# Optimization experiments

Measured on AMD Instinct MI355X. Metric: run time of the kernel, lower is better.

Reference implementation:

```python
import jax, jax.numpy as jnp
import numpy as np

B, T, D, Q = 32, 2048, 512, 512


def setup_inputs() -> dict:
    key = jax.random.key(0)
    k0, k1, k2, k3, k4, k5 = jax.random.split(key, 6)
    output_data = jax.random.normal(k0, (B, T, D), dtype=jnp.float32)
    query = jax.random.normal(k1, (B, Q), dtype=jnp.float32)
    # valid lengths in [1, T] so no row is fully masked
    lengths = jax.random.randint(k2, (B,), 1, T + 1).astype(jnp.int32)
    w = jax.random.normal(k3, (D, D), dtype=jnp.float32) * (1.0 / np.sqrt(D))
    u = jax.random.normal(k4, (D, Q), dtype=jnp.float32) * (1.0 / np.sqrt(Q))
    v = jax.random.normal(k5, (D, 1), dtype=jnp.float32)
    return {"output_data": output_data, "query": query, "lengths": lengths,
            "w": w, "u": u, "v": v}


def reference(output_data, query, lengths, w, u, v):
    # raw_score = W @ output + U @ query (broadcast over seq)   [B, T, D]
    raw = jnp.einsum('btd,ed->bte', output_data, w) \
        + jnp.einsum('bq,eq->be', query, u)[:, None, :]
    # score = tanh(raw) @ v                                     [B, T, 1]
    score = jnp.tanh(raw) @ v
    # additive mask: 0 on valid positions, -inf on padding
    valid = jnp.arange(T)[None, :] < lengths[:, None]           # [B, T]
    score = score + jnp.where(valid, 0.0, -jnp.inf)[:, :, None]
    weights = jax.nn.softmax(score, axis=1)                     # [B, T, 1]
    expectation = jnp.sum(weights * output_data, axis=1)        # [B, D]
    # dropout_rate=0.0 -> dropout is identity
    return score, weights, expectation
```

## Files before the change

kernel.cpp:

```cpp
#include <hip/hip_runtime.h>
#include <math.h>


#define TPB 256
constexpr int B = 32, T = 2048, D = 512, Qd = 512;
constexpr int NROW = B * T;
#define NEG_SENTINEL (-1e30f)

typedef __attribute__((ext_vector_type(8))) short bf16x8;
typedef __attribute__((ext_vector_type(4))) float f32x4;

__device__ __forceinline__ unsigned rne16(float f) {
    unsigned u = __builtin_bit_cast(unsigned, f);
    return (u + 0x7FFFu + ((u >> 16) & 1u)) >> 16;
}
__device__ __forceinline__ unsigned packsplit(float f0, float f1, unsigned& lopack) {
    unsigned h0 = rne16(f0), h1 = rne16(f1);
    float r0 = f0 - __builtin_bit_cast(float, h0 << 16);
    float r1 = f1 - __builtin_bit_cast(float, h1 << 16);
    lopack = rne16(r0) | (rne16(r1) << 16);
    return h0 | (h1 << 16);
}
__device__ __forceinline__ void cvt8(const float4 a, const float4 b, uint4& hi, uint4& lo) {
    hi.x = packsplit(a.x, a.y, lo.x);
    hi.y = packsplit(a.z, a.w, lo.y);
    hi.z = packsplit(b.x, b.y, lo.z);
    hi.w = packsplit(b.z, b.w, lo.w);
}

__global__ void k_uq(const float* __restrict__ query, const float* __restrict__ u,
                     float* __restrict__ uq) {
    int b = blockIdx.x;
    __shared__ float q_s[Qd];
    for (int i = threadIdx.x; i < Qd; i += TPB) q_s[i] = query[b * Qd + i];
    __syncthreads();
    for (int e = threadIdx.x; e < D; e += TPB) {
        const float4* urow = (const float4*)(u + (size_t)e * Qd);
        float acc = 0.f;
        for (int q4 = 0; q4 < Qd / 4; ++q4) {
            float4 uu = urow[q4];
            float4 qq = *(const float4*)(q_s + q4 * 4);
            acc += uu.x * qq.x + uu.y * qq.y + uu.z * qq.z + uu.w * qq.w;
        }
        uq[b * D + e] = acc;
    }
}

__global__ void k_convW(const float* __restrict__ W,
                        uint4* __restrict__ WhF, uint4* __restrict__ WlF) {
    const int g = blockIdx.x * 256 + threadIdx.x;
    const int e = g >> 6, s = g & 63;
    const float4* src = (const float4*)(W + (size_t)e * D + s * 8);
    float4 a = src[0], bq = src[1];
    uint4 hi, lo;
    cvt8(a, bq, hi, lo);
    const int nt = e >> 7, cb = (e >> 4) & 7, lo16 = e & 15;
    const int kc = s >> 2, hi4 = s & 3;
    const size_t idx = ((size_t)(nt * 16 + kc) * 8 + cb) * 64 + hi4 * 16 + lo16;
    WhF[idx] = hi;
    WlF[idx] = lo;
}

__global__ __launch_bounds__(256, 2) void k_gemm(
    const float* __restrict__ X,
    const uint4* __restrict__ WhF,
    const uint4* __restrict__ WlF,
    const float* __restrict__ v,
    const float* __restrict__ uqg,
    float* __restrict__ partialS)
{
    __shared__ uint4 Ah[4 * 128], Al[4 * 128];
    __shared__ float scr[2][128];

    const int gidx = blockIdx.x;
    const int logical = (gidx & 7) * 256 + (gidx >> 3);
    const int mt = logical >> 2, nt = logical & 3;
    const int row0 = mt * 128, e0 = nt * 128;
    const int b = row0 >> 11;

    const int tid = threadIdx.x, lane = tid & 63, wid = tid >> 6;
    const int wm = wid >> 1, wn = wid & 1;
    const int lo16 = lane & 15, hi4 = lane >> 4;
    const int arow = tid & 127, akh = tid >> 7;

    const float4* Xg = (const float4*)(X + (size_t)(row0 + arow) * D + akh * 16);
    const uint4* WhB = WhF + ((size_t)nt * 16) * 8 * 64 + (wn * 4) * 64 + lane;
    const uint4* WlB = WlF + ((size_t)nt * 16) * 8 * 64 + (wn * 4) * 64 + lane;

    f32x4 acc[4][4];
#pragma unroll
    for (int i = 0; i < 4; ++i)
#pragma unroll
        for (int j = 0; j < 4; ++j) acc[i][j] = (f32x4){0.f, 0.f, 0.f, 0.f};

    float4 xr0 = Xg[0], xr1 = Xg[1], xr2 = Xg[2], xr3 = Xg[3];

    for (int kc = 0; kc < 16; ++kc) {
        __syncthreads();
        uint4 bhr[4], blr[4];
        {
            const uint4* wh = WhB + (size_t)kc * 8 * 64;
            const uint4* wl = WlB + (size_t)kc * 8 * 64;
#pragma unroll
            for (int fc = 0; fc < 4; ++fc) {
                bhr[fc] = wh[fc * 64];
                blr[fc] = wl[fc * 64];
            }
        }
        {
            uint4 hp, lp;
            cvt8(xr0, xr1, hp, lp);
            Ah[(akh * 2 + 0) * 128 + arow] = hp;
            Al[(akh * 2 + 0) * 128 + arow] = lp;
            cvt8(xr2, xr3, hp, lp);
            Ah[(akh * 2 + 1) * 128 + arow] = hp;
            Al[(akh * 2 + 1) * 128 + arow] = lp;
        }
        __syncthreads();

        bf16x8 aH[4], aL[4];
#pragma unroll
        for (int fr = 0; fr < 4; ++fr) {
            const int idx = hi4 * 128 + wm * 64 + fr * 16 + lo16;
            aH[fr] = __builtin_bit_cast(bf16x8, Ah[idx]);
            aL[fr] = __builtin_bit_cast(bf16x8, Al[idx]);
        }
        if (kc + 1 < 16) {
            const float4* xn = Xg + (size_t)(kc + 1) * 8;
            xr0 = xn[0]; xr1 = xn[1]; xr2 = xn[2]; xr3 = xn[3];
        }
#pragma unroll
        for (int fc = 0; fc < 4; ++fc) {
            const bf16x8 bH = __builtin_bit_cast(bf16x8, bhr[fc]);
            const bf16x8 bL = __builtin_bit_cast(bf16x8, blr[fc]);
#pragma unroll
            for (int fr = 0; fr < 4; ++fr) {
                acc[fr][fc] = __builtin_amdgcn_mfma_f32_16x16x32_bf16(aH[fr], bH, acc[fr][fc], 0, 0, 0);
                acc[fr][fc] = __builtin_amdgcn_mfma_f32_16x16x32_bf16(aH[fr], bL, acc[fr][fc], 0, 0, 0);
                acc[fr][fc] = __builtin_amdgcn_mfma_f32_16x16x32_bf16(aL[fr], bH, acc[fr][fc], 0, 0, 0);
            }
        }
    }

    const int colbase = e0 + wn * 64;
#pragma unroll
    for (int fr = 0; fr < 4; ++fr) {
        float ps[4] = {0.f, 0.f, 0.f, 0.f};
#pragma unroll
        for (int fc = 0; fc < 4; ++fc) {
            const int col = colbase + fc * 16 + lo16;
            const float uqc = uqg[b * D + col];
            const float vc  = v[col];
#pragma unroll
            for (int i = 0; i < 4; ++i)
                ps[i] += tanhf(acc[fr][fc][i] + uqc) * vc;
        }
#pragma unroll
        for (int i = 0; i < 4; ++i) {
            float p = ps[i];
#pragma unroll
            for (int off = 8; off >= 1; off >>= 1) p += __shfl_xor(p, off, 16);
            if (lo16 == 0) scr[wn][wm * 64 + fr * 16 + hi4 * 4 + i] = p;
        }
    }
    __syncthreads();
    if (tid < 128)
        partialS[(size_t)nt * NROW + row0 + tid] = scr[0][tid] + scr[1][tid];
}

__global__ void k_combine(const float* __restrict__ partialS,
                          const int* __restrict__ lengths,
                          float* __restrict__ score) {
    const int i = blockIdx.x * TPB + threadIdx.x;
    const int b = i >> 11, t = i & (T - 1);
    float s = partialS[i] + partialS[NROW + i] + partialS[2 * NROW + i] + partialS[3 * NROW + i];
    score[i] = (t < lengths[b]) ? s : NEG_SENTINEL;
}

__global__ void k_softmax(const float* __restrict__ score, float* __restrict__ weights) {
    const int b = blockIdx.x;
    const float* s = score + (size_t)b * T;
    float m = -INFINITY;
    for (int t = threadIdx.x; t < T; t += TPB) m = fmaxf(m, s[t]);
#pragma unroll
    for (int off = 32; off >= 1; off >>= 1) m = fmaxf(m, __shfl_xor(m, off, 64));
    __shared__ float redm[4];
    if ((threadIdx.x & 63) == 0) redm[threadIdx.x >> 6] = m;
    __syncthreads();
    m = fmaxf(fmaxf(redm[0], redm[1]), fmaxf(redm[2], redm[3]));

    float sum = 0.f;
    for (int t = threadIdx.x; t < T; t += TPB) sum += __expf(s[t] - m);
#pragma unroll
    for (int off = 32; off >= 1; off >>= 1) sum += __shfl_xor(sum, off, 64);
    __shared__ float reds[4];
    if ((threadIdx.x & 63) == 0) reds[threadIdx.x >> 6] = sum;
    __syncthreads();
    const float inv = 1.f / (reds[0] + reds[1] + reds[2] + reds[3]);

    for (int t = threadIdx.x; t < T; t += TPB)
        weights[(size_t)b * T + t] = __expf(s[t] - m) * inv;
}

__global__ void k_exp_partial(const float* __restrict__ X, const float* __restrict__ wts,
                              float* __restrict__ part) {
    const int b = blockIdx.x >> 4;
    const int c = blockIdx.x & 15;
    const int t0 = c * 128;
    const int d0 = threadIdx.x * 4;
    const float* Xb = X + ((size_t)b * T + t0) * D + d0;
    const float* wb = wts + (size_t)b * T + t0;
    float4 a = {0.f, 0.f, 0.f, 0.f};
    for (int t = 0; t < 128; ++t) {
        const float wgt = wb[t];
        const float4 x = *(const float4*)(Xb + (size_t)t * D);
        a.x += wgt * x.x; a.y += wgt * x.y; a.z += wgt * x.z; a.w += wgt * x.w;
    }
    *(float4*)(part + ((size_t)(b * 16 + c)) * D + d0) = a;
}

__global__ void k_exp_reduce(const float* __restrict__ part, float* __restrict__ out) {
    const int i = blockIdx.x * TPB + threadIdx.x;
    const int b = i >> 9, d = i & 511;
    float a = 0.f;
#pragma unroll
    for (int c = 0; c < 16; ++c) a += part[((size_t)(b * 16 + c)) * D + d];
    out[i] = a;
}

extern "C" void kernel_launch(void* const* d_in, const int* in_sizes, int n_in,
                              void* d_out, int out_size, void* d_ws, size_t ws_size,
                              hipStream_t stream) {
    const float* X      = (const float*)d_in[0];
    const float* query  = (const float*)d_in[1];
    const int*   len    = (const int*)  d_in[2];
    const float* w      = (const float*)d_in[3];
    const float* u      = (const float*)d_in[4];
    const float* v      = (const float*)d_in[5];

    float* out     = (float*)d_out;
    float* score   = out;
    float* weights = out + (size_t)B * T;
    float* expec   = out + (size_t)2 * B * T;

    float* uq       = (float*)d_ws;
    float* partialS = uq + (size_t)B * D;
    uint4* WhF      = (uint4*)(partialS + (size_t)4 * NROW);
    uint4* WlF      = WhF + 32768;
    float* part     = partialS;

    k_uq         <<<B,            TPB, 0, stream>>>(query, u, uq);
    k_convW      <<<128,          TPB, 0, stream>>>(w, WhF, WlF);
    k_gemm       <<<2048,         TPB, 0, stream>>>(X, WhF, WlF, v, uq, partialS);
    k_combine    <<<NROW / TPB,   TPB, 0, stream>>>(partialS, len, score);
    k_softmax    <<<B,            TPB, 0, stream>>>(score, weights);
    k_exp_partial<<<B * 16,       128, 0, stream>>>(X, weights, part);
    k_exp_reduce <<<B * D / TPB,  TPB, 0, stream>>>(part, expec);
}
```

Baseline: 200.5 us.

## Double-buffer A tile in LDS, prefetch X two chunks ahead, use fast tanh

The GEMM kernel now keeps two LDS buffers for the split bf16 A tile. It converts and stores the next chunk while MFMAs run on the current one, so each k-iteration needs only one barrier instead of two. X is prefetched into registers two chunks ahead. The launch bounds are raised to allow three blocks per CU, and tanhf is replaced with an exp-based formula. In exchange, LDS use doubles, register pressure rises (with possible spills under the tighter bound), and tanh accuracy drops slightly.

```diff
diff --git a/kernel.cpp b/kernel.cpp
--- a/kernel.cpp
+++ b/kernel.cpp
@@ -26,6 +26,12 @@
     hi.y = packsplit(a.z, a.w, lo.y);
     hi.z = packsplit(b.x, b.y, lo.z);
     hi.w = packsplit(b.z, b.w, lo.w);
+}
+__device__ __forceinline__ float fast_tanh(float x) {
+    float a = fabsf(x);
+    float e = __expf(-2.f * a);
+    float t = (1.f - e) / (1.f + e);
+    return copysignf(t, x);
 }
 
 __global__ void k_uq(const float* __restrict__ query, const float* __restrict__ u,
@@ -61,7 +67,7 @@
     WlF[idx] = lo;
 }
 
-__global__ __launch_bounds__(256, 2) void k_gemm(
+__global__ __launch_bounds__(256, 3) void k_gemm(
     const float* __restrict__ X,
     const uint4* __restrict__ WhF,
     const uint4* __restrict__ WlF,
@@ -69,7 +75,7 @@
     const float* __restrict__ uqg,
     float* __restrict__ partialS)
 {
-    __shared__ uint4 Ah[4 * 128], Al[4 * 128];
+    __shared__ uint4 Ah[2][4 * 128], Al[2][4 * 128];
     __shared__ float scr[2][128];
 
     const int gidx = blockIdx.x;
@@ -93,10 +99,26 @@
 #pragma unroll
         for (int j = 0; j < 4; ++j) acc[i][j] = (f32x4){0.f, 0.f, 0.f, 0.f};
 
-    float4 xr0 = Xg[0], xr1 = Xg[1], xr2 = Xg[2], xr3 = Xg[3];
-
+    float4 xr[2][4];
+#pragma unroll
+    for (int i = 0; i < 4; ++i) xr[0][i] = Xg[i];
+#pragma unroll
+    for (int i = 0; i < 4; ++i) xr[1][i] = Xg[8 + i];
+    {
+        uint4 hp, lp;
+        cvt8(xr[0][0], xr[0][1], hp, lp);
+        Ah[0][(akh * 2 + 0) * 128 + arow] = hp;
+        Al[0][(akh * 2 + 0) * 128 + arow] = lp;
+        cvt8(xr[0][2], xr[0][3], hp, lp);
+        Ah[0][(akh * 2 + 1) * 128 + arow] = hp;
+        Al[0][(akh * 2 + 1) * 128 + arow] = lp;
+    }
+
+#pragma unroll
     for (int kc = 0; kc < 16; ++kc) {
+        const int cur = kc & 1, nxt = cur ^ 1;
         __syncthreads();
+
         uint4 bhr[4], blr[4];
         {
             const uint4* wh = WhB + (size_t)kc * 8 * 64;
@@ -107,28 +129,25 @@
                 blr[fc] = wl[fc * 64];
             }
         }
-        {
+
+        if (kc + 1 < 16) {
             uint4 hp, lp;
-            cvt8(xr0, xr1, hp, lp);
-            Ah[(akh * 2 + 0) * 128 + arow] = hp;
-            Al[(akh * 2 + 0) * 128 + arow] = lp;
-            cvt8(xr2, xr3, hp, lp);
-            Ah[(akh * 2 + 1) * 128 + arow] = hp;
-            Al[(akh * 2 + 1) * 128 + arow] = lp;
-        }
-        __syncthreads();
+            cvt8(xr[nxt][0], xr[nxt][1], hp, lp);
+            Ah[nxt][(akh * 2 + 0) * 128 + arow] = hp;
+            Al[nxt][(akh * 2 + 0) * 128 + arow] = lp;
+            cvt8(xr[nxt][2], xr[nxt][3], hp, lp);
+            Ah[nxt][(akh * 2 + 1) * 128 + arow] = hp;
+            Al[nxt][(akh * 2 + 1) * 128 + arow] = lp;
+        }
 
         bf16x8 aH[4], aL[4];
 #pragma unroll
         for (int fr = 0; fr < 4; ++fr) {
             const int idx = hi4 * 128 + wm * 64 + fr * 16 + lo16;
-            aH[fr] = __builtin_bit_cast(bf16x8, Ah[idx]);
-            aL[fr] = __builtin_bit_cast(bf16x8, Al[idx]);
-        }
-        if (kc + 1 < 16) {
-            const float4* xn = Xg + (size_t)(kc + 1) * 8;
-            xr0 = xn[0]; xr1 = xn[1]; xr2 = xn[2]; xr3 = xn[3];
-        }
+            aH[fr] = __builtin_bit_cast(bf16x8, Ah[cur][idx]);
+            aL[fr] = __builtin_bit_cast(bf16x8, Al[cur][idx]);
+        }
+
 #pragma unroll
         for (int fc = 0; fc < 4; ++fc) {
             const bf16x8 bH = __builtin_bit_cast(bf16x8, bhr[fc]);
@@ -140,6 +159,11 @@
                 acc[fr][fc] = __builtin_amdgcn_mfma_f32_16x16x32_bf16(aL[fr], bH, acc[fr][fc], 0, 0, 0);
             }
         }
+
+        if (kc + 2 < 16) {
+#pragma unroll
+            for (int i = 0; i < 4; ++i) xr[cur][i] = Xg[(kc + 2) * 8 + i];
+        }
     }
 
     const int colbase = e0 + wn * 64;
@@ -153,7 +177,7 @@
             const float vc  = v[col];
 #pragma unroll
             for (int i = 0; i < 4; ++i)
-                ps[i] += tanhf(acc[fr][fc][i] + uqc) * vc;
+                ps[i] += fast_tanh(acc[fr][fc][i] + uqc) * vc;
         }
 #pragma unroll
         for (int i = 0; i < 4; ++i) {
```

Result: faster. 196.6 us, median of 2 (-2.0%).

## Load A fragments directly from global into registers, drop LDS staging; fast tanh

Applied to the files above, without the earlier changes.

The GEMM kernel no longer stages the bf16 hi/lo split of X through shared memory with two barriers per k-step. Each wave now loads its own A fragment rows straight from global memory and converts them in registers, double-buffering both A and B loads one k-step ahead. The epilogue also swaps tanhf for an exp-based fast tanh. Each A element is now loaded and converted by both column-half waves (wn), which doubles global load traffic and conversion work and raises register pressure.

```diff
diff --git a/kernel.cpp b/kernel.cpp
--- a/kernel.cpp
+++ b/kernel.cpp
@@ -21,11 +21,11 @@
     lopack = rne16(r0) | (rne16(r1) << 16);
     return h0 | (h1 << 16);
 }
-__device__ __forceinline__ void cvt8(const float4 a, const float4 b, uint4& hi, uint4& lo) {
-    hi.x = packsplit(a.x, a.y, lo.x);
-    hi.y = packsplit(a.z, a.w, lo.y);
-    hi.z = packsplit(b.x, b.y, lo.z);
-    hi.w = packsplit(b.z, b.w, lo.w);
+__device__ __forceinline__ float fast_tanh(float x) {
+    float a = fabsf(x);
+    float e = __expf(-2.f * a);
+    float t = (1.f - e) / (1.f + e);
+    return copysignf(t, x);
 }
 
 __global__ void k_uq(const float* __restrict__ query, const float* __restrict__ u,
@@ -53,7 +53,10 @@
     const float4* src = (const float4*)(W + (size_t)e * D + s * 8);
     float4 a = src[0], bq = src[1];
     uint4 hi, lo;
-    cvt8(a, bq, hi, lo);
+    hi.x = packsplit(a.x, a.y, lo.x);
+    hi.y = packsplit(a.z, a.w, lo.y);
+    hi.z = packsplit(bq.x, bq.y, lo.z);
+    hi.w = packsplit(bq.z, bq.w, lo.w);
     const int nt = e >> 7, cb = (e >> 4) & 7, lo16 = e & 15;
     const int kc = s >> 2, hi4 = s & 3;
     const size_t idx = ((size_t)(nt * 16 + kc) * 8 + cb) * 64 + hi4 * 16 + lo16;
@@ -69,7 +72,6 @@
     const float* __restrict__ uqg,
     float* __restrict__ partialS)
 {
-    __shared__ uint4 Ah[4 * 128], Al[4 * 128];
     __shared__ float scr[2][128];
 
     const int gidx = blockIdx.x;
@@ -81,9 +83,8 @@
     const int tid = threadIdx.x, lane = tid & 63, wid = tid >> 6;
     const int wm = wid >> 1, wn = wid & 1;
     const int lo16 = lane & 15, hi4 = lane >> 4;
-    const int arow = tid & 127, akh = tid >> 7;
-
-    const float4* Xg = (const float4*)(X + (size_t)(row0 + arow) * D + akh * 16);
+
+    const float* Xb = X + (size_t)(row0 + wm * 64 + lo16) * D + hi4 * 8;
     const uint4* WhB = WhF + ((size_t)nt * 16) * 8 * 64 + (wn * 4) * 64 + lane;
     const uint4* WlB = WlF + ((size_t)nt * 16) * 8 * 64 + (wn * 4) * 64 + lane;
 
@@ -93,54 +94,65 @@
 #pragma unroll
         for (int j = 0; j < 4; ++j) acc[i][j] = (f32x4){0.f, 0.f, 0.f, 0.f};
 
-    float4 xr0 = Xg[0], xr1 = Xg[1], xr2 = Xg[2], xr3 = Xg[3];
+    float4 xa[4], xb[4];
+    uint4 bh[4], bl[4];
+
+#define LOAD_A(KC)                                                          \
+    {                                                                        \
+        _Pragma("unroll")                                                    \
+        for (int fr = 0; fr < 4; ++fr) {                                     \
+            const float* p = Xb + (size_t)fr * 16 * D + (KC) * 32;           \
+            xa[fr] = *(const float4*)p;                                      \
+            xb[fr] = *(const float4*)(p + 4);                                \
+        }                                                                    \
+    }
+#define LOAD_B(KC)                                                          \
+    {                                                                        \
+        const uint4* wh = WhB + (size_t)(KC) * 8 * 64;                       \
+        const uint4* wl = WlB + (size_t)(KC) * 8 * 64;                       \
+        _Pragma("unroll")                                                    \
+        for (int fc = 0; fc < 4; ++fc) {                                     \
+            bh[fc] = wh[fc * 64];                                            \
+            bl[fc] = wl[fc * 64];                                            \
+        }                                                                    \
+    }
+
+    LOAD_A(0)
+    LOAD_B(0)
 
     for (int kc = 0; kc < 16; ++kc) {
-        __syncthreads();
-        uint4 bhr[4], blr[4];
-        {
-            const uint4* wh = WhB + (size_t)kc * 8 * 64;
-            const uint4* wl = WlB + (size_t)kc * 8 * 64;
-#pragma unroll
-            for (int fc = 0; fc < 4; ++fc) {
-                bhr[fc] = wh[fc * 64];
-                blr[fc] = wl[fc * 64];
+        bf16x8 aH[4], aL[4];
+#pragma unroll
+        for (int fr = 0; fr < 4; ++fr) {
+            uint4 h, l;
+            h.x = packsplit(xa[fr].x, xa[fr].y, l.x);
+            h.y = packsplit(xa[fr].z, xa[fr].w, l.y);
+            h.z = packsplit(xb[fr].x, xb[fr].y, l.z);
+            h.w = packsplit(xb[fr].z, xb[fr].w, l.w);
+            aH[fr] = __builtin_bit_cast(bf16x8, h);
+            aL[fr] = __builtin_bit_cast(bf16x8, l);
+        }
+        bf16x8 bH[4], bL[4];
+#pragma unroll
+        for (int fc = 0; fc < 4; ++fc) {
+            bH[fc] = __builtin_bit_cast(bf16x8, bh[fc]);
+            bL[fc] = __builtin_bit_cast(bf16x8, bl[fc]);
+        }
+        if (kc + 1 < 16) {
+            LOAD_A(kc + 1)
+            LOAD_B(kc + 1)
+        }
+#pragma unroll
+        for (int fc = 0; fc < 4; ++fc)
+#pragma unroll
+            for (int fr = 0; fr < 4; ++fr) {
+                acc[fr][fc] = __builtin_amdgcn_mfma_f32_16x16x32_bf16(aH[fr], bH[fc], acc[fr][fc], 0, 0, 0);
+                acc[fr][fc] = __builtin_amdgcn_mfma_f32_16x16x32_bf16(aH[fr], bL[fc], acc[fr][fc], 0, 0, 0);
+                acc[fr][fc] = __builtin_amdgcn_mfma_f32_16x16x32_bf16(aL[fr], bH[fc], acc[fr][fc], 0, 0, 0);
             }
-        }
-        {
-            uint4 hp, lp;
-            cvt8(xr0, xr1, hp, lp);
-            Ah[(akh * 2 + 0) * 128 + arow] = hp;
-            Al[(akh * 2 + 0) * 128 + arow] = lp;
-            cvt8(xr2, xr3, hp, lp);
-            Ah[(akh * 2 + 1) * 128 + arow] = hp;
-            Al[(akh * 2 + 1) * 128 + arow] = lp;
-        }
-        __syncthreads();
-
-        bf16x8 aH[4], aL[4];
-#pragma unroll
-        for (int fr = 0; fr < 4; ++fr) {
-            const int idx = hi4 * 128 + wm * 64 + fr * 16 + lo16;
-            aH[fr] = __builtin_bit_cast(bf16x8, Ah[idx]);
-            aL[fr] = __builtin_bit_cast(bf16x8, Al[idx]);
-        }
-        if (kc + 1 < 16) {
-            const float4* xn = Xg + (size_t)(kc + 1) * 8;
-            xr0 = xn[0]; xr1 = xn[1]; xr2 = xn[2]; xr3 = xn[3];
-        }
-#pragma unroll
-        for (int fc = 0; fc < 4; ++fc) {
-            const bf16x8 bH = __builtin_bit_cast(bf16x8, bhr[fc]);
-            const bf16x8 bL = __builtin_bit_cast(bf16x8, blr[fc]);
-#pragma unroll
-            for (int fr = 0; fr < 4; ++fr) {
-                acc[fr][fc] = __builtin_amdgcn_mfma_f32_16x16x32_bf16(aH[fr], bH, acc[fr][fc], 0, 0, 0);
-                acc[fr][fc] = __builtin_amdgcn_mfma_f32_16x16x32_bf16(aH[fr], bL, acc[fr][fc], 0, 0, 0);
-                acc[fr][fc] = __builtin_amdgcn_mfma_f32_16x16x32_bf16(aL[fr], bH, acc[fr][fc], 0, 0, 0);
-            }
-        }
-    }
+    }
+#undef LOAD_A
+#undef LOAD_B
 
     const int colbase = e0 + wn * 64;
 #pragma unroll
@@ -153,7 +165,7 @@
             const float vc  = v[col];
 #pragma unroll
             for (int i = 0; i < 4; ++i)
-                ps[i] += tanhf(acc[fr][fc][i] + uqc) * vc;
+                ps[i] += fast_tanh(acc[fr][fc][i] + uqc) * vc;
         }
 #pragma unroll
         for (int i = 0; i < 4; ++i) {
```

After: 243.4 us. +21.4%, slower.
